# Performance work log

Measured on AMD Instinct MI355X. Metric: run time of the kernel, lower is better.

The kernel has to match this reference:

```python
import jax, jax.numpy as jnp
import numpy as np

B, N, D, H, K = 4, 256, 128, 8, 16

def setup_inputs() -> dict:
    key = jax.random.key(0)
    ks = jax.random.split(key, 6)
    h = jax.random.normal(ks[0], (B, N, D), jnp.float32)
    e_att = jax.random.normal(ks[1], (B, N, N, H, K), jnp.float32)
    e_val = jax.random.normal(ks[2], (B, N, N, H, K), jnp.float32)
    mask = jnp.ones((B, N), jnp.float32)
    scale = 1.0 / np.sqrt(D).astype(np.float32)
    Wq = jax.random.normal(ks[3], (D, H * K), jnp.float32) * scale
    Wk = jax.random.normal(ks[4], (D, H * K), jnp.float32) * scale
    Wv = jax.random.normal(ks[5], (D, H * K), jnp.float32) * scale
    return {"h": h, "e_att": e_att, "e_val": e_val, "mask": mask, "Wq": Wq, "Wk": Wk, "Wv": Wv}

def reference(h, e_att, e_val, mask, Wq, Wk, Wv):
    b, n, _ = h.shape
    Q = (h @ Wq).reshape(b, n, H, K)
    Kh = (h @ Wk).reshape(b, n, H, K) * (float(K) ** -0.5)
    V = (h @ Wv).reshape(b, n, H, K)
    # (b,i,j,h) dot-product scores, broadcast over k, plus per-edge bias
    scores = jnp.einsum('bihk,bjhk->bijh', Q, Kh)[..., None] + e_att
    scores = jnp.exp(jnp.clip(scores, -5.0, 5.0))
    attn_mask = mask[:, :, None, None, None] * mask[:, None, :, None, None]
    scores = scores * attn_mask
    softmax_denom = jnp.maximum(scores.sum(axis=2), 1e-6)  # (b,i,h,k)
    scores = scores * attn_mask  # dropout p=0 -> identity on mask
    out = jnp.einsum('bijhk,bjhk->bihk', scores, V)
    out = out + (scores * e_val).sum(axis=2)
    out = out / softmax_denom
    return out.reshape(b, n, H * K)
```

## Files before the change

### kernel.cpp

```cpp
#include <hip/hip_runtime.h>
#include <hip/hip_bf16.h>

#define Bb 4
#define Nn 256
#define Dd 128
#define Hh 8
#define Kk 16
#define HK 128
#define BN 1024

__global__ __launch_bounds__(128) void qkv_kernel(
    const float* __restrict__ h,
    const float* __restrict__ Wq,
    const float* __restrict__ Wk,
    const float* __restrict__ Wv,
    float* __restrict__ Qw, float* __restrict__ Kw, float* __restrict__ Vw)
{
    __shared__ float hrows[8][Dd];
    const int rb = blockIdx.x;
    const int t  = threadIdx.x;
    #pragma unroll
    for (int r = 0; r < 8; ++r)
        hrows[r][t] = h[(size_t)(rb * 8 + r) * Dd + t];
    __syncthreads();

    float aq[8], ak[8], av[8];
    #pragma unroll
    for (int r = 0; r < 8; ++r) { aq[r] = 0.f; ak[r] = 0.f; av[r] = 0.f; }

    for (int d = 0; d < Dd; ++d) {
        const float wq = Wq[d * HK + t];
        const float wk = Wk[d * HK + t];
        const float wv = Wv[d * HK + t];
        #pragma unroll
        for (int r = 0; r < 8; ++r) {
            const float hv = hrows[r][d];
            aq[r] = fmaf(hv, wq, aq[r]);
            ak[r] = fmaf(hv, wk, ak[r]);
            av[r] = fmaf(hv, wv, av[r]);
        }
    }
    #pragma unroll
    for (int r = 0; r < 8; ++r) {
        const size_t o = (size_t)(rb * 8 + r) * HK + t;
        Qw[o] = aq[r];
        Kw[o] = ak[r] * 0.25f;
        Vw[o] = av[r];
    }
}

#define QKP 9

__global__ __launch_bounds__(512) void attn_kernel(
    const float* __restrict__ e_att,
    const float* __restrict__ e_val,
    const float* __restrict__ mask,
    const float* __restrict__ Qw,
    const float* __restrict__ Kw,
    const float* __restrict__ Vw,
    float* __restrict__ out)
{
    __shared__ float qrow[HK];
    __shared__ float mrow[Nn];
    __shared__ float qk_s[Nn * QKP];
    __shared__ float red[3 * 16 * HK];

    const int t  = threadIdx.x;
    const int bi = blockIdx.x;
    const int b  = bi >> 8;

    if (t < HK) qrow[t] = Qw[(size_t)bi * HK + t];
    if (t < Nn) mrow[t] = mask[b * Nn + t];
    __syncthreads();

    const float maski = mrow[bi & 255];

    {
        const int j    = t >> 1;
        const int half = t & 1;
        const float4* kp = (const float4*)(Kw + (size_t)(b * Nn + j) * HK + half * 64);
        const float*  qp = qrow + half * 64;
        #pragma unroll
        for (int hl = 0; hl < 4; ++hl) {
            const float4 k0 = kp[hl * 4 + 0], k1 = kp[hl * 4 + 1];
            const float4 k2 = kp[hl * 4 + 2], k3 = kp[hl * 4 + 3];
            const float* q = qp + hl * Kk;
            float acc = 0.f;
            acc = fmaf(q[0],  k0.x, acc); acc = fmaf(q[1],  k0.y, acc);
            acc = fmaf(q[2],  k0.z, acc); acc = fmaf(q[3],  k0.w, acc);
            acc = fmaf(q[4],  k1.x, acc); acc = fmaf(q[5],  k1.y, acc);
            acc = fmaf(q[6],  k1.z, acc); acc = fmaf(q[7],  k1.w, acc);
            acc = fmaf(q[8],  k2.x, acc); acc = fmaf(q[9],  k2.y, acc);
            acc = fmaf(q[10], k2.z, acc); acc = fmaf(q[11], k2.w, acc);
            acc = fmaf(q[12], k3.x, acc); acc = fmaf(q[13], k3.y, acc);
            acc = fmaf(q[14], k3.z, acc); acc = fmaf(q[15], k3.w, acc);
            qk_s[j * QKP + half * 4 + hl] = acc;
        }
    }
    __syncthreads();

    const int q32  = t & 31;
    const int joff = t >> 5;
    const int hk4  = q32 * 4;
    const int hh   = q32 >> 2;

    float acc_d[4] = {0,0,0,0}, acc_v[4] = {0,0,0,0}, acc_e[4] = {0,0,0,0};
    const size_t slice = (size_t)bi * (Nn * HK);
    const float* vbase = Vw + (size_t)(b * Nn) * HK;

#define LOADSET(EA, EV, VV, JB) do {                                         \
        const int j_ = (JB) + joff;                                          \
        const size_t eo_ = slice + (size_t)j_ * HK + hk4;                    \
        EA = *(const float4*)(e_att + eo_);                                  \
        EV = *(const float4*)(e_val + eo_);                                  \
        VV = *(const float4*)(vbase + (size_t)j_ * HK + hk4);                \
    } while (0)

#define COMPUTE(EA, EV, VV, JB) do {                                         \
        const int j_ = (JB) + joff;                                          \
        const float qk_ = qk_s[j_ * QKP + hh];                               \
        const float m_  = maski * mrow[j_];                                  \
        const float m2_ = m_ * m_;                                           \
        const float eaf_[4] = {EA.x, EA.y, EA.z, EA.w};                      \
        const float evf_[4] = {EV.x, EV.y, EV.z, EV.w};                      \
        const float vvf_[4] = {VV.x, VV.y, VV.z, VV.w};                      \
        _Pragma("unroll")                                                    \
        for (int l = 0; l < 4; ++l) {                                        \
            float x_ = qk_ + eaf_[l];                                        \
            x_ = fminf(fmaxf(x_, -5.f), 5.f);                                \
            const float e_ = __expf(x_);                                     \
            acc_d[l] = fmaf(e_, m_, acc_d[l]);                               \
            const float s2_ = e_ * m2_;                                      \
            acc_v[l] = fmaf(s2_, vvf_[l], acc_v[l]);                         \
            acc_e[l] = fmaf(s2_, evf_[l], acc_e[l]);                         \
        }                                                                    \
    } while (0)

    float4 eaA, evA, vvA, eaB, evB, vvB;
    LOADSET(eaA, evA, vvA, 0);
    LOADSET(eaB, evB, vvB, 16);

    #pragma unroll
    for (int k = 0; k < 7; ++k) {
        const int jb = k * 32;
        COMPUTE(eaA, evA, vvA, jb);
        LOADSET(eaA, evA, vvA, jb + 32);
        COMPUTE(eaB, evB, vvB, jb + 16);
        LOADSET(eaB, evB, vvB, jb + 48);
    }
    COMPUTE(eaA, evA, vvA, 224);
    COMPUTE(eaB, evB, vvB, 240);

#undef LOADSET
#undef COMPUTE

    __syncthreads();

    #pragma unroll
    for (int l = 0; l < 4; ++l) {
        red[0 * 2048 + joff * HK + hk4 + l] = acc_d[l];
        red[1 * 2048 + joff * HK + hk4 + l] = acc_v[l];
        red[2 * 2048 + joff * HK + hk4 + l] = acc_e[l];
    }
    __syncthreads();

    if (t < HK) {
        float D = 0.f, OV = 0.f, OE = 0.f;
        #pragma unroll
        for (int p = 0; p < 16; ++p) {
            D  += red[0 * 2048 + p * HK + t];
            OV += red[1 * 2048 + p * HK + t];
            OE += red[2 * 2048 + p * HK + t];
        }
        out[(size_t)bi * HK + t] = (OV + OE) / fmaxf(D, 1e-6f);
    }
}

extern "C" void kernel_launch(void* const* d_in, const int* in_sizes, int n_in,
                              void* d_out, int out_size, void* d_ws, size_t ws_size,
                              hipStream_t stream) {
    const float* h     = (const float*)d_in[0];
    const float* e_att = (const float*)d_in[1];
    const float* e_val = (const float*)d_in[2];
    const float* mask  = (const float*)d_in[3];
    const float* Wq    = (const float*)d_in[4];
    const float* Wk    = (const float*)d_in[5];
    const float* Wv    = (const float*)d_in[6];
    float* out = (float*)d_out;

    float* Qw  = (float*)d_ws;
    float* Kw  = Qw + (size_t)BN * HK;
    float* Vw  = Kw + (size_t)BN * HK;

    qkv_kernel<<<128, 128, 0, stream>>>(h, Wq, Wk, Wv, Qw, Kw, Vw);
    attn_kernel<<<BN, 512, 0, stream>>>(e_att, e_val, mask, Qw, Kw, Vw, out);
}
```

Baseline: 73.62 us.

## Use nontemporal edge loads, remap attention blocks, and widen QKV grid

Edge tensors e_att and e_val are now read with nontemporal loads, since they are streamed exactly once and should not evict the reused K/V rows from cache. Attention block indices are permuted so that consecutively launched blocks fall in different batches, which changes how K/V reuse spreads across XCDs and L2. The QKV projection now handles 2 rows per block instead of 8 and launches 512 blocks, with 8-deep weight prefetch, to fill more CUs. The price is more redundant weight reads per output row.

```diff
diff --git a/kernel.cpp b/kernel.cpp
--- a/kernel.cpp
+++ b/kernel.cpp
@@ -9,6 +9,15 @@
 #define HK 128
 #define BN 1024
 
+typedef float vf4 __attribute__((ext_vector_type(4)));
+
+__device__ __forceinline__ vf4 ntload4(const float* p) {
+    return __builtin_nontemporal_load((const vf4*)p);
+}
+__device__ __forceinline__ vf4 ld4(const float* p) {
+    return *(const vf4*)p;
+}
+
 __global__ __launch_bounds__(128) void qkv_kernel(
     const float* __restrict__ h,
     const float* __restrict__ Wq,
@@ -16,37 +25,36 @@
     const float* __restrict__ Wv,
     float* __restrict__ Qw, float* __restrict__ Kw, float* __restrict__ Vw)
 {
-    __shared__ float hrows[8][Dd];
+    __shared__ float hrows[2][Dd];
     const int rb = blockIdx.x;
     const int t  = threadIdx.x;
-    #pragma unroll
-    for (int r = 0; r < 8; ++r)
-        hrows[r][t] = h[(size_t)(rb * 8 + r) * Dd + t];
-    __syncthreads();
-
-    float aq[8], ak[8], av[8];
-    #pragma unroll
-    for (int r = 0; r < 8; ++r) { aq[r] = 0.f; ak[r] = 0.f; av[r] = 0.f; }
-
-    for (int d = 0; d < Dd; ++d) {
-        const float wq = Wq[d * HK + t];
-        const float wk = Wk[d * HK + t];
-        const float wv = Wv[d * HK + t];
-        #pragma unroll
-        for (int r = 0; r < 8; ++r) {
-            const float hv = hrows[r][d];
-            aq[r] = fmaf(hv, wq, aq[r]);
-            ak[r] = fmaf(hv, wk, ak[r]);
-            av[r] = fmaf(hv, wv, av[r]);
-        }
-    }
-    #pragma unroll
-    for (int r = 0; r < 8; ++r) {
-        const size_t o = (size_t)(rb * 8 + r) * HK + t;
-        Qw[o] = aq[r];
-        Kw[o] = ak[r] * 0.25f;
-        Vw[o] = av[r];
-    }
+    hrows[0][t] = h[(size_t)(rb * 2 + 0) * Dd + t];
+    hrows[1][t] = h[(size_t)(rb * 2 + 1) * Dd + t];
+    __syncthreads();
+
+    float aq0 = 0.f, aq1 = 0.f, ak0 = 0.f, ak1 = 0.f, av0 = 0.f, av1 = 0.f;
+    for (int d0 = 0; d0 < Dd; d0 += 8) {
+        float wq[8], wk[8], wv[8];
+        #pragma unroll
+        for (int u = 0; u < 8; ++u) {
+            wq[u] = Wq[(d0 + u) * HK + t];
+            wk[u] = Wk[(d0 + u) * HK + t];
+            wv[u] = Wv[(d0 + u) * HK + t];
+        }
+        #pragma unroll
+        for (int u = 0; u < 8; ++u) {
+            const float h0 = hrows[0][d0 + u];
+            const float h1 = hrows[1][d0 + u];
+            aq0 = fmaf(h0, wq[u], aq0); aq1 = fmaf(h1, wq[u], aq1);
+            ak0 = fmaf(h0, wk[u], ak0); ak1 = fmaf(h1, wk[u], ak1);
+            av0 = fmaf(h0, wv[u], av0); av1 = fmaf(h1, wv[u], av1);
+        }
+    }
+    const size_t o0 = (size_t)(rb * 2 + 0) * HK + t;
+    const size_t o1 = (size_t)(rb * 2 + 1) * HK + t;
+    Qw[o0] = aq0;          Qw[o1] = aq1;
+    Kw[o0] = ak0 * 0.25f;  Kw[o1] = ak1 * 0.25f;
+    Vw[o0] = av0;          Vw[o1] = av1;
 }
 
 #define QKP 9
@@ -66,7 +74,7 @@
     __shared__ float red[3 * 16 * HK];
 
     const int t  = threadIdx.x;
-    const int bi = blockIdx.x;
+    const int bi = ((blockIdx.x & 7) << 7) | (blockIdx.x >> 3);
     const int b  = bi >> 8;
 
     if (t < HK) qrow[t] = Qw[(size_t)bi * HK + t];
@@ -78,12 +86,12 @@
     {
         const int j    = t >> 1;
         const int half = t & 1;
-        const float4* kp = (const float4*)(Kw + (size_t)(b * Nn + j) * HK + half * 64);
+        const float*  kb = Kw + (size_t)(b * Nn + j) * HK + half * 64;
         const float*  qp = qrow + half * 64;
         #pragma unroll
         for (int hl = 0; hl < 4; ++hl) {
-            const float4 k0 = kp[hl * 4 + 0], k1 = kp[hl * 4 + 1];
-            const float4 k2 = kp[hl * 4 + 2], k3 = kp[hl * 4 + 3];
+            const vf4 k0 = ld4(kb + hl * 16 + 0), k1 = ld4(kb + hl * 16 + 4);
+            const vf4 k2 = ld4(kb + hl * 16 + 8), k3 = ld4(kb + hl * 16 + 12);
             const float* q = qp + hl * Kk;
             float acc = 0.f;
             acc = fmaf(q[0],  k0.x, acc); acc = fmaf(q[1],  k0.y, acc);
@@ -111,9 +119,9 @@
 #define LOADSET(EA, EV, VV, JB) do {                                         \
         const int j_ = (JB) + joff;                                          \
         const size_t eo_ = slice + (size_t)j_ * HK + hk4;                    \
-        EA = *(const float4*)(e_att + eo_);                                  \
-        EV = *(const float4*)(e_val + eo_);                                  \
-        VV = *(const float4*)(vbase + (size_t)j_ * HK + hk4);                \
+        EA = ntload4(e_att + eo_);                                           \
+        EV = ntload4(e_val + eo_);                                           \
+        VV = ld4(vbase + (size_t)j_ * HK + hk4);                             \
     } while (0)
 
 #define COMPUTE(EA, EV, VV, JB) do {                                         \
@@ -136,7 +144,7 @@
         }                                                                    \
     } while (0)
 
-    float4 eaA, evA, vvA, eaB, evB, vvB;
+    vf4 eaA, evA, vvA, eaB, evB, vvB;
     LOADSET(eaA, evA, vvA, 0);
     LOADSET(eaB, evB, vvB, 16);
 
@@ -192,6 +200,6 @@
     float* Kw  = Qw + (size_t)BN * HK;
     float* Vw  = Kw + (size_t)BN * HK;
 
-    qkv_kernel<<<128, 128, 0, stream>>>(h, Wq, Wk, Wv, Qw, Kw, Vw);
+    qkv_kernel<<<512, 128, 0, stream>>>(h, Wq, Wk, Wv, Qw, Kw, Vw);
     attn_kernel<<<BN, 512, 0, stream>>>(e_att, e_val, mask, Qw, Kw, Vw, out);
 }
```

Result: no change. 72.72 us (-1.2%).
